# Kernel optimization log

Measured on AMD Instinct MI355X. Metric: run time of the kernel, lower is better.

## Reference

```python
import jax, jax.numpy as jnp
import numpy as np

KS = (3, 3)   # kernel_size
ST = (1, 1)   # stride
PD = (1, 1)   # padding
EPS = 1e-5


def unfold(x):
    """im2col matching torch.nn.Unfold: [B,C,H,W] -> [B, C*kh*kw, L] with (c,kh,kw) channel order, L row-major."""
    kh, kw = KS; sh, sw = ST; ph, pw = PD
    x = jnp.pad(x, ((0, 0), (0, 0), (ph, ph), (pw, pw)))
    B, C, H, W = x.shape
    Ho = (H - kh) // sh + 1
    Wo = (W - kw) // sw + 1
    I = (jnp.arange(Ho) * sh)[:, None, None, None] + jnp.arange(kh)[None, :, None, None]
    J = (jnp.arange(Wo) * sw)[None, None, :, None] + jnp.arange(kw)[None, None, None, :]
    p = x[:, :, I, J]  # [B, C, Ho, kh, Wo, kw]
    return p.transpose(0, 1, 3, 5, 2, 4).reshape(B, C * kh * kw, Ho * Wo)


def fold(cols, x_shape):
    """torch.nn.Fold is exactly the adjoint of Unfold (overlap-add)."""
    _, vjp = jax.vjp(unfold, jnp.zeros(x_shape, cols.dtype))
    return vjp(cols)[0]


def setup_inputs() -> dict:
    key = jax.random.key(0)
    k = jax.random.split(key, 6)
    B, C, H, W = 16, 64, 64, 64
    Cout, K = 64, KS[0] * KS[1]
    return {
        "x_mag": jax.random.uniform(k[0], (B, C, H, W), jnp.float32),
        "x_ang": jax.random.normal(k[1], (B, C, H, W), jnp.float32),
        "w_mag": jax.random.uniform(k[2], (C, K), jnp.float32),
        "w_ang": jax.random.uniform(k[3], (C, K), jnp.float32),
        "w1": jax.random.uniform(k[4], (C, K), jnp.float32),
        "w2": jax.random.uniform(k[5], (Cout, C), jnp.float32),
    }


def reference(x_mag, x_ang, w_mag, w_ang, w1, w2):
    B, C, H, W = x_mag.shape
    K = KS[0] * KS[1]
    Cout = w2.shape[0]
    Ho = (H + 2 * PD[0] - KS[0]) // ST[0] + 1
    Wo = (W + 2 * PD[1] - KS[1]) // ST[1] + 1

    # outer layer: unfold, mix with normalized weights, fold back (overlap-add)
    nws_mag = w_mag ** 2 / jnp.sum(w_mag ** 2)   # _normalize_weights_squared
    nw_ang = w_ang / jnp.sum(w_ang ** 2)         # _normalize_weights
    cm = unfold(x_mag).reshape(B, C, K, -1) + nws_mag[None, :, :, None]
    ca = unfold(x_ang).reshape(B, C, K, -1) * nw_ang[None, :, :, None]
    fm = fold(cm.reshape(B, C * K, -1), (B, C, H, W))
    fa = fold(ca.reshape(B, C * K, -1), (B, C, H, W))

    # helper: second unfold + weighted Frechet-mean reduction
    tbm = unfold(fm).reshape(B, C, K, -1)  # [B,C,K,L]
    tba = unfold(fa).reshape(B, C, K, -1)
    wmm1 = w1 ** 2 / jnp.sum(w1 ** 2, axis=1, keepdims=True)  # row-normalized
    wmm2 = w2 ** 2 / jnp.sum(w2 ** 2, axis=1, keepdims=True)
    wma1 = w1 ** 2 / jnp.sum(w1 ** 2)                          # globally normalized
    wma2 = w2 ** 2 / jnp.sum(w2 ** 2)

    m1 = jnp.einsum('bckl,ck->bcl', jnp.log(tbm + EPS), wmm1)
    out_mag = jnp.exp(jnp.einsum('bcl,oc->bol', m1, wmm2)).reshape(B, Cout, Ho, Wo)
    a1 = jnp.einsum('bckl,ck->bcl', tba, wma1)
    out_ang = jnp.einsum('bcl,oc->bol', a1, wma2).reshape(B, Cout, Ho, Wo)

    # from_polar -> stack (real, imag) on axis 1
    return jnp.stack([out_mag * jnp.cos(out_ang), out_mag * jnp.sin(out_ang)], axis=1)
```

## Files before the change

### kernel.cpp

```cpp
#include <hip/hip_runtime.h>
#include <math.h>

#define NB 16
#define NC 64
#define NL 4096
#define NCOUT 64
#define EPSF 1e-5f
#define LOG_EPSF -11.512925464970229f
#define CC 8
#define NCHUNK 8

#define FMA16(ACC, MV, W) \
  (ACC)[0].x = fmaf((MV).x,(W).x,(ACC)[0].x); (ACC)[0].y = fmaf((MV).y,(W).x,(ACC)[0].y); \
  (ACC)[0].z = fmaf((MV).z,(W).x,(ACC)[0].z); (ACC)[0].w = fmaf((MV).w,(W).x,(ACC)[0].w); \
  (ACC)[1].x = fmaf((MV).x,(W).y,(ACC)[1].x); (ACC)[1].y = fmaf((MV).y,(W).y,(ACC)[1].y); \
  (ACC)[1].z = fmaf((MV).z,(W).y,(ACC)[1].z); (ACC)[1].w = fmaf((MV).w,(W).y,(ACC)[1].w); \
  (ACC)[2].x = fmaf((MV).x,(W).z,(ACC)[2].x); (ACC)[2].y = fmaf((MV).y,(W).z,(ACC)[2].y); \
  (ACC)[2].z = fmaf((MV).z,(W).z,(ACC)[2].z); (ACC)[2].w = fmaf((MV).w,(W).z,(ACC)[2].w); \
  (ACC)[3].x = fmaf((MV).x,(W).w,(ACC)[3].x); (ACC)[3].y = fmaf((MV).y,(W).w,(ACC)[3].y); \
  (ACC)[3].z = fmaf((MV).z,(W).w,(ACC)[3].z); (ACC)[3].w = fmaf((MV).w,(W).w,(ACC)[3].w);

__global__ __launch_bounds__(512, 4) void fused_kernel(
    const float* __restrict__ x_mag, const float* __restrict__ x_ang,
    const float* __restrict__ wm, const float* __restrict__ wa,
    const float* __restrict__ w1, const float* __restrict__ w2,
    float* __restrict__ out)
{
    __shared__ __align__(16) float lfm[CC][4][72];
    __shared__ __align__(16) float fas[CC][4][72];
    __shared__ __align__(16) float m1r[2][CC][2][64];
    __shared__ __align__(16) float a1r[2][CC][2][64];
    __shared__ __align__(16) float w2m[64][68];
    __shared__ float wm1s[64][9], wa1s[64][9];
    __shared__ float smag_s[64][9], tang_s[64][9];
    __shared__ float red[4][8];
    __shared__ __align__(16) float rho[64];

    const int tid  = threadIdx.x;
    const int lane = tid & 63;
    const int wv   = tid >> 6;

    const int bid = (blockIdx.x & 7) * 64 + (blockIdx.x >> 3);
    const int b  = bid >> 5;
    const int i0 = (bid & 31) * 2;

    const int sr = lane >> 4;
    const int j4 = lane & 15;
    const int ir = i0 - 1 + sr;
    const bool ok = ((unsigned)ir < 64u);
    const int irc = ok ? ir : 0;
    const int ci = (ir == 0) ? 0 : ((ir == 63) ? 2 : 1);
    const int kL = ci * 3 + 0, kC = ci * 3 + 1, kR = ci * 3 + 2;
    const float ni = (ci == 1) ? 3.f : 2.f;
    const float nCt = 3.f * ni;
    const float n0 = (j4 == 0)  ? 2.f * ni : nCt;
    const float n3 = (j4 == 15) ? 2.f * ni : nCt;

    const float* spm = x_mag + ((size_t)(b * NC + wv) * NL + irc * 64 + j4 * 4);
    const float* spa = x_ang + ((size_t)(b * NC + wv) * NL + irc * 64 + j4 * 4);

    float4 pfm = *(const float4*)spm;
    float4 pfa = *(const float4*)spa;

    const int mrr = tid >> 8;
    const int o0  = ((tid >> 4) & 15) * 4;
    const int l0  = (tid & 15) * 4;

    float p0 = 0.f, p1 = 0.f, p2 = 0.f;
    {
        float v;
        v = wm[tid]; p0 += v * v;
        v = wa[tid]; p1 += v * v;
        v = w1[tid]; p2 += v * v;
        if (tid < 64) {
            v = wm[tid + 512]; p0 += v * v;
            v = wa[tid + 512]; p1 += v * v;
            v = w1[tid + 512]; p2 += v * v;
        }
    }
    #pragma unroll
    for (int s = 32; s; s >>= 1) {
        p0 += __shfl_down(p0, s); p1 += __shfl_down(p1, s); p2 += __shfl_down(p2, s);
    }
    if (lane == 0) { red[0][wv] = p0; red[1][wv] = p1; red[2][wv] = p2; }

    float sqv[2][4], r2v[2][4];
    float s22p = 0.f;
    #pragma unroll
    for (int k = 0; k < 2; ++k) {
        const int oq = wv + 8 * k;
        #pragma unroll
        for (int n = 0; n < 4; ++n) {
            float v = w2[(oq * 4 + n) * 64 + lane];
            float s = v * v;
            sqv[k][n] = s;
            float rr_ = s;
            rr_ += __shfl_xor(rr_, 1);  rr_ += __shfl_xor(rr_, 2);
            rr_ += __shfl_xor(rr_, 4);  rr_ += __shfl_xor(rr_, 8);
            rr_ += __shfl_xor(rr_, 16); rr_ += __shfl_xor(rr_, 32);
            r2v[k][n] = rr_;
        }
        s22p += r2v[k][0] + r2v[k][1] + r2v[k][2] + r2v[k][3];
    }
    if (lane == 0) red[3][wv] = s22p;
    __syncthreads();
    const float s_wm2 = red[0][0] + red[0][1] + red[0][2] + red[0][3]
                      + red[0][4] + red[0][5] + red[0][6] + red[0][7];
    const float s_wa2 = red[1][0] + red[1][1] + red[1][2] + red[1][3]
                      + red[1][4] + red[1][5] + red[1][6] + red[1][7];
    const float s_w12 = red[2][0] + red[2][1] + red[2][2] + red[2][3]
                      + red[2][4] + red[2][5] + red[2][6] + red[2][7];
    const float inv_s22 = 1.f / (red[3][0] + red[3][1] + red[3][2] + red[3][3]
                               + red[3][4] + red[3][5] + red[3][6] + red[3][7]);

    #pragma unroll
    for (int k = 0; k < 2; ++k) {
        const int oq = wv + 8 * k;
        float4 wmv4;
        wmv4.x = sqv[k][0] / r2v[k][0];
        wmv4.y = sqv[k][1] / r2v[k][1];
        wmv4.z = sqv[k][2] / r2v[k][2];
        wmv4.w = sqv[k][3] / r2v[k][3];
        *(float4*)&w2m[lane][oq * 4] = wmv4;
        if (lane == 0) {
            rho[oq * 4 + 0] = r2v[k][0] * inv_s22;
            rho[oq * 4 + 1] = r2v[k][1] * inv_s22;
            rho[oq * 4 + 2] = r2v[k][2] * inv_s22;
            rho[oq * 4 + 3] = r2v[k][3] * inv_s22;
        }
    }

    if (tid < 64) {
        const int c = tid;
        float q[9]; float r1c = 0.f;
        #pragma unroll
        for (int k = 0; k < 9; ++k) { float v = w1[c * 9 + k]; q[k] = v * v; r1c += q[k]; }
        float inv_r = 1.f / r1c, inv_s = 1.f / s_w12;
        #pragma unroll
        for (int k = 0; k < 9; ++k) { wm1s[c][k] = q[k] * inv_r; wa1s[c][k] = q[k] * inv_s; }
    } else if (tid < 128) {
        const int c = tid - 64;
        float nm[9], na[9];
        const float inv_m = 1.f / s_wm2, inv_a = 1.f / s_wa2;
        #pragma unroll
        for (int k = 0; k < 9; ++k) {
            float v = wm[c * 9 + k];
            nm[k] = v * v * inv_m;
            na[k] = wa[c * 9 + k] * inv_a;
        }
        #pragma unroll
        for (int ci_ = 0; ci_ < 3; ++ci_) {
            #pragma unroll
            for (int cj = 0; cj < 3; ++cj) {
                float sm = 0.f, sa = 0.f;
                #pragma unroll
                for (int ki = 0; ki < 3; ++ki) {
                    bool vi = (ci_ == 0) ? (ki < 2) : ((ci_ == 2) ? (ki > 0) : true);
                    if (!vi) continue;
                    #pragma unroll
                    for (int kj = 0; kj < 3; ++kj) {
                        bool vj = (cj == 0) ? (kj < 2) : ((cj == 2) ? (kj > 0) : true);
                        if (!vj) continue;
                        sm += nm[ki * 3 + kj];
                        sa += na[ki * 3 + kj];
                    }
                }
                smag_s[c][ci_ * 3 + cj] = sm;
                tang_s[c][ci_ * 3 + cj] = sa;
            }
        }
    }
    __syncthreads();

    float4 accm[4], acca[4];
    #pragma unroll
    for (int oi = 0; oi < 4; ++oi) {
        accm[oi].x = accm[oi].y = accm[oi].z = accm[oi].w = 0.f;
        acca[oi].x = acca[oi].y = acca[oi].z = acca[oi].w = 0.f;
    }

    auto do_matmul = [&](int chm, int pp) {
        const int c0 = chm * CC;
        #pragma unroll
        for (int cc = 0; cc < CC; ++cc) {
            float4 mv  = *(const float4*)&m1r[pp][cc][mrr][l0];
            float4 av  = *(const float4*)&a1r[pp][cc][mrr][l0];
            float4 wmv = *(const float4*)&w2m[c0 + cc][o0];
            FMA16(accm, mv, wmv);
            FMA16(acca, av, wmv);
        }
    };

    #pragma unroll 2
    for (int ch = 0; ch < NCHUNK; ++ch) {
        const int p = ch & 1;
        const int cg = ch * CC + wv;

        {
            float4 dm, da;
            if (ok) {
                float sC = smag_s[cg][kC], tC = tang_s[cg][kC];
                float s0 = (j4 == 0)  ? smag_s[cg][kL] : sC;
                float s3 = (j4 == 15) ? smag_s[cg][kR] : sC;
                float t0 = (j4 == 0)  ? tang_s[cg][kL] : tC;
                float t3 = (j4 == 15) ? tang_s[cg][kR] : tC;
                dm.x = __logf(fmaf(n0,  pfm.x, s0) + EPSF);
                dm.y = __logf(fmaf(nCt, pfm.y, sC) + EPSF);
                dm.z = __logf(fmaf(nCt, pfm.z, sC) + EPSF);
                dm.w = __logf(fmaf(n3,  pfm.w, s3) + EPSF);
                da.x = pfa.x * t0; da.y = pfa.y * tC;
                da.z = pfa.z * tC; da.w = pfa.w * t3;
            } else {
                dm.x = dm.y = dm.z = dm.w = LOG_EPSF;
                da.x = da.y = da.z = da.w = 0.f;
            }
            *(float4*)&lfm[wv][sr][4 + j4 * 4] = dm;
            *(float4*)&fas[wv][sr][4 + j4 * 4] = da;
            if (j4 == 0)  { lfm[wv][sr][3]  = LOG_EPSF; fas[wv][sr][3]  = 0.f; }
            if (j4 == 15) { lfm[wv][sr][68] = LOG_EPSF; fas[wv][sr][68] = 0.f; }
        }

        if (ch + 1 < NCHUNK) {
            pfm = *(const float4*)(spm + (size_t)(ch + 1) * CC * NL);
            pfa = *(const float4*)(spa + (size_t)(ch + 1) * CC * NL);
        }

        if (ch > 0) do_matmul(ch - 1, p ^ 1);

        {
            float mres0 = 0.f, mres1 = 0.f, ares0 = 0.f, ares1 = 0.f;
            #pragma unroll
            for (int r_ = 0; r_ < 4; ++r_) {
                float l0v = lfm[wv][r_][lane + 3];
                float l1v = lfm[wv][r_][lane + 4];
                float l2v = lfm[wv][r_][lane + 5];
                float a0v = fas[wv][r_][lane + 3];
                float a1v = fas[wv][r_][lane + 4];
                float a2v = fas[wv][r_][lane + 5];
                if (r_ < 3) {
                    mres0 = fmaf(wm1s[cg][r_ * 3 + 0], l0v, mres0);
                    mres0 = fmaf(wm1s[cg][r_ * 3 + 1], l1v, mres0);
                    mres0 = fmaf(wm1s[cg][r_ * 3 + 2], l2v, mres0);
                    ares0 = fmaf(wa1s[cg][r_ * 3 + 0], a0v, ares0);
                    ares0 = fmaf(wa1s[cg][r_ * 3 + 1], a1v, ares0);
                    ares0 = fmaf(wa1s[cg][r_ * 3 + 2], a2v, ares0);
                }
                if (r_ > 0) {
                    const int ki = r_ - 1;
                    mres1 = fmaf(wm1s[cg][ki * 3 + 0], l0v, mres1);
                    mres1 = fmaf(wm1s[cg][ki * 3 + 1], l1v, mres1);
                    mres1 = fmaf(wm1s[cg][ki * 3 + 2], l2v, mres1);
                    ares1 = fmaf(wa1s[cg][ki * 3 + 0], a0v, ares1);
                    ares1 = fmaf(wa1s[cg][ki * 3 + 1], a1v, ares1);
                    ares1 = fmaf(wa1s[cg][ki * 3 + 2], a2v, ares1);
                }
            }
            m1r[p][wv][0][lane] = mres0;
            m1r[p][wv][1][lane] = mres1;
            a1r[p][wv][0][lane] = ares0;
            a1r[p][wv][1][lane] = ares1;
        }
        __syncthreads();
    }
    do_matmul(NCHUNK - 1, 1);

    const float4 rh4 = *(const float4*)&rho[o0];
    acca[0].x *= rh4.x; acca[0].y *= rh4.x; acca[0].z *= rh4.x; acca[0].w *= rh4.x;
    acca[1].x *= rh4.y; acca[1].y *= rh4.y; acca[1].z *= rh4.y; acca[1].w *= rh4.y;
    acca[2].x *= rh4.z; acca[2].y *= rh4.z; acca[2].z *= rh4.z; acca[2].w *= rh4.z;
    acca[3].x *= rh4.w; acca[3].y *= rh4.w; acca[3].z *= rh4.w; acca[3].w *= rh4.w;

    #pragma unroll
    for (int oi = 0; oi < 4; ++oi) {
        float4 am = accm[oi], aa = acca[oi];
        float4 oc, os;
        float ex;
        ex = __expf(am.x); oc.x = ex * __cosf(aa.x); os.x = ex * __sinf(aa.x);
        ex = __expf(am.y); oc.y = ex * __cosf(aa.y); os.y = ex * __sinf(aa.y);
        ex = __expf(am.z); oc.z = ex * __cosf(aa.z); os.z = ex * __sinf(aa.z);
        ex = __expf(am.w); oc.w = ex * __cosf(aa.w); os.w = ex * __sinf(aa.w);
        size_t gi = ((size_t)(b * 2) * NCOUT + o0 + oi) * NL + (size_t)(i0 + mrr) * 64 + l0;
        *(float4*)&out[gi] = oc;
        *(float4*)&out[gi + (size_t)NCOUT * NL] = os;
    }
}

extern "C" void kernel_launch(void* const* d_in, const int* in_sizes, int n_in,
                              void* d_out, int out_size, void* d_ws, size_t ws_size,
                              hipStream_t stream) {
    const float* x_mag = (const float*)d_in[0];
    const float* x_ang = (const float*)d_in[1];
    const float* w_mag = (const float*)d_in[2];
    const float* w_ang = (const float*)d_in[3];
    const float* w1    = (const float*)d_in[4];
    const float* w2    = (const float*)d_in[5];
    float* out = (float*)d_out;

    fused_kernel<<<NB * 32, 512, 0, stream>>>(x_mag, x_ang, w_mag, w_ang, w1, w2, out);
}
```

Measured before the change: 42.59 us.

## Process one output row per block with 256 threads and raise matmul wave priority

```diff
diff --git a/kernel.cpp b/kernel.cpp
--- a/kernel.cpp
+++ b/kernel.cpp
@@ -7,8 +7,8 @@
 #define NCOUT 64
 #define EPSF 1e-5f
 #define LOG_EPSF -11.512925464970229f
-#define CC 8
-#define NCHUNK 8
+#define CC 4
+#define NCHUNK 16
 
 #define FMA16(ACC, MV, W) \
   (ACC)[0].x = fmaf((MV).x,(W).x,(ACC)[0].x); (ACC)[0].y = fmaf((MV).y,(W).x,(ACC)[0].y); \
@@ -20,34 +20,35 @@
   (ACC)[3].x = fmaf((MV).x,(W).w,(ACC)[3].x); (ACC)[3].y = fmaf((MV).y,(W).w,(ACC)[3].y); \
   (ACC)[3].z = fmaf((MV).z,(W).w,(ACC)[3].z); (ACC)[3].w = fmaf((MV).w,(W).w,(ACC)[3].w);
 
-__global__ __launch_bounds__(512, 4) void fused_kernel(
+__global__ __launch_bounds__(256, 4) void fused_kernel(
     const float* __restrict__ x_mag, const float* __restrict__ x_ang,
     const float* __restrict__ wm, const float* __restrict__ wa,
     const float* __restrict__ w1, const float* __restrict__ w2,
     float* __restrict__ out)
 {
-    __shared__ __align__(16) float lfm[CC][4][72];
-    __shared__ __align__(16) float fas[CC][4][72];
-    __shared__ __align__(16) float m1r[2][CC][2][64];
-    __shared__ __align__(16) float a1r[2][CC][2][64];
+    __shared__ __align__(16) float lfm[CC][3][72];
+    __shared__ __align__(16) float fas[CC][3][72];
+    __shared__ __align__(16) float m1r[2][CC][64];
+    __shared__ __align__(16) float a1r[2][CC][64];
     __shared__ __align__(16) float w2m[64][68];
     __shared__ float wm1s[64][9], wa1s[64][9];
     __shared__ float smag_s[64][9], tang_s[64][9];
-    __shared__ float red[4][8];
+    __shared__ float red[4][4];
     __shared__ __align__(16) float rho[64];
 
     const int tid  = threadIdx.x;
     const int lane = tid & 63;
     const int wv   = tid >> 6;
 
-    const int bid = (blockIdx.x & 7) * 64 + (blockIdx.x >> 3);
-    const int b  = bid >> 5;
-    const int i0 = (bid & 31) * 2;
+    const int bid = (blockIdx.x & 7) * 128 + (blockIdx.x >> 3);
+    const int b  = bid >> 6;
+    const int iy = bid & 63;
 
     const int sr = lane >> 4;
     const int j4 = lane & 15;
-    const int ir = i0 - 1 + sr;
-    const bool ok = ((unsigned)ir < 64u);
+    const bool act = (sr < 3);
+    const int ir = iy - 1 + sr;
+    const bool ok = act && ((unsigned)ir < 64u);
     const int irc = ok ? ir : 0;
     const int ci = (ir == 0) ? 0 : ((ir == 63) ? 2 : 1);
     const int kL = ci * 3 + 0, kC = ci * 3 + 1, kR = ci * 3 + 2;
@@ -59,19 +60,18 @@
     const float* spm = x_mag + ((size_t)(b * NC + wv) * NL + irc * 64 + j4 * 4);
     const float* spa = x_ang + ((size_t)(b * NC + wv) * NL + irc * 64 + j4 * 4);
 
-    float4 pfm = *(const float4*)spm;
-    float4 pfa = *(const float4*)spa;
-
-    const int mrr = tid >> 8;
-    const int o0  = ((tid >> 4) & 15) * 4;
-    const int l0  = (tid & 15) * 4;
+    float4 pfm, pfa;
+    if (act) { pfm = *(const float4*)spm; pfa = *(const float4*)spa; }
+
+    const int o0 = (tid >> 4) * 4;
+    const int l0 = (tid & 15) * 4;
 
     float p0 = 0.f, p1 = 0.f, p2 = 0.f;
     {
         float v;
-        v = wm[tid]; p0 += v * v;
-        v = wa[tid]; p1 += v * v;
-        v = w1[tid]; p2 += v * v;
+        v = wm[tid];       p0 += v * v;  v = wm[tid + 256]; p0 += v * v;
+        v = wa[tid];       p1 += v * v;  v = wa[tid + 256]; p1 += v * v;
+        v = w1[tid];       p2 += v * v;  v = w1[tid + 256]; p2 += v * v;
         if (tid < 64) {
             v = wm[tid + 512]; p0 += v * v;
             v = wa[tid + 512]; p1 += v * v;
@@ -84,11 +84,11 @@
     }
     if (lane == 0) { red[0][wv] = p0; red[1][wv] = p1; red[2][wv] = p2; }
 
-    float sqv[2][4], r2v[2][4];
+    float sqv[4][4], r2v[4][4];
     float s22p = 0.f;
     #pragma unroll
-    for (int k = 0; k < 2; ++k) {
-        const int oq = wv + 8 * k;
+    for (int k = 0; k < 4; ++k) {
+        const int oq = wv + 4 * k;
         #pragma unroll
         for (int n = 0; n < 4; ++n) {
             float v = w2[(oq * 4 + n) * 64 + lane];
@@ -104,18 +104,14 @@
     }
     if (lane == 0) red[3][wv] = s22p;
     __syncthreads();
-    const float s_wm2 = red[0][0] + red[0][1] + red[0][2] + red[0][3]
-                      + red[0][4] + red[0][5] + red[0][6] + red[0][7];
-    const float s_wa2 = red[1][0] + red[1][1] + red[1][2] + red[1][3]
-                      + red[1][4] + red[1][5] + red[1][6] + red[1][7];
-    const float s_w12 = red[2][0] + red[2][1] + red[2][2] + red[2][3]
-                      + red[2][4] + red[2][5] + red[2][6] + red[2][7];
-    const float inv_s22 = 1.f / (red[3][0] + red[3][1] + red[3][2] + red[3][3]
-                               + red[3][4] + red[3][5] + red[3][6] + red[3][7]);
-
-    #pragma unroll
-    for (int k = 0; k < 2; ++k) {
-        const int oq = wv + 8 * k;
+    const float s_wm2 = red[0][0] + red[0][1] + red[0][2] + red[0][3];
+    const float s_wa2 = red[1][0] + red[1][1] + red[1][2] + red[1][3];
+    const float s_w12 = red[2][0] + red[2][1] + red[2][2] + red[2][3];
+    const float inv_s22 = 1.f / (red[3][0] + red[3][1] + red[3][2] + red[3][3]);
+
+    #pragma unroll
+    for (int k = 0; k < 4; ++k) {
+        const int oq = wv + 4 * k;
         float4 wmv4;
         wmv4.x = sqv[k][0] / r2v[k][0];
         wmv4.y = sqv[k][1] / r2v[k][1];
@@ -181,14 +177,16 @@
 
     auto do_matmul = [&](int chm, int pp) {
         const int c0 = chm * CC;
+        __builtin_amdgcn_s_setprio(1);
         #pragma unroll
         for (int cc = 0; cc < CC; ++cc) {
-            float4 mv  = *(const float4*)&m1r[pp][cc][mrr][l0];
-            float4 av  = *(const float4*)&a1r[pp][cc][mrr][l0];
+            float4 mv  = *(const float4*)&m1r[pp][cc][l0];
+            float4 av  = *(const float4*)&a1r[pp][cc][l0];
             float4 wmv = *(const float4*)&w2m[c0 + cc][o0];
             FMA16(accm, mv, wmv);
             FMA16(acca, av, wmv);
         }
+        __builtin_amdgcn_s_setprio(0);
     };
 
     #pragma unroll 2
@@ -196,7 +194,7 @@
         const int p = ch & 1;
         const int cg = ch * CC + wv;
 
-        {
+        if (act) {
             float4 dm, da;
             if (ok) {
                 float sC = smag_s[cg][kC], tC = tang_s[cg][kC];
@@ -220,7 +218,7 @@
             if (j4 == 15) { lfm[wv][sr][68] = LOG_EPSF; fas[wv][sr][68] = 0.f; }
         }
 
-        if (ch + 1 < NCHUNK) {
+        if (act && (ch + 1 < NCHUNK)) {
             pfm = *(const float4*)(spm + (size_t)(ch + 1) * CC * NL);
             pfa = *(const float4*)(spa + (size_t)(ch + 1) * CC * NL);
         }
@@ -228,37 +226,18 @@
         if (ch > 0) do_matmul(ch - 1, p ^ 1);
 
         {
-            float mres0 = 0.f, mres1 = 0.f, ares0 = 0.f, ares1 = 0.f;
+            float mres = 0.f, ares = 0.f;
             #pragma unroll
-            for (int r_ = 0; r_ < 4; ++r_) {
-                float l0v = lfm[wv][r_][lane + 3];
-                float l1v = lfm[wv][r_][lane + 4];
-                float l2v = lfm[wv][r_][lane + 5];
-                float a0v = fas[wv][r_][lane + 3];
-                float a1v = fas[wv][r_][lane + 4];
-                float a2v = fas[wv][r_][lane + 5];
-                if (r_ < 3) {
-                    mres0 = fmaf(wm1s[cg][r_ * 3 + 0], l0v, mres0);
-                    mres0 = fmaf(wm1s[cg][r_ * 3 + 1], l1v, mres0);
-                    mres0 = fmaf(wm1s[cg][r_ * 3 + 2], l2v, mres0);
-                    ares0 = fmaf(wa1s[cg][r_ * 3 + 0], a0v, ares0);
-                    ares0 = fmaf(wa1s[cg][r_ * 3 + 1], a1v, ares0);
-                    ares0 = fmaf(wa1s[cg][r_ * 3 + 2], a2v, ares0);
-                }
-                if (r_ > 0) {
-                    const int ki = r_ - 1;
-                    mres1 = fmaf(wm1s[cg][ki * 3 + 0], l0v, mres1);
-                    mres1 = fmaf(wm1s[cg][ki * 3 + 1], l1v, mres1);
-                    mres1 = fmaf(wm1s[cg][ki * 3 + 2], l2v, mres1);
-                    ares1 = fmaf(wa1s[cg][ki * 3 + 0], a0v, ares1);
-                    ares1 = fmaf(wa1s[cg][ki * 3 + 1], a1v, ares1);
-                    ares1 = fmaf(wa1s[cg][ki * 3 + 2], a2v, ares1);
-                }
+            for (int r_ = 0; r_ < 3; ++r_) {
+                mres = fmaf(wm1s[cg][r_ * 3 + 0], lfm[wv][r_][lane + 3], mres);
+                mres = fmaf(wm1s[cg][r_ * 3 + 1], lfm[wv][r_][lane + 4], mres);
+                mres = fmaf(wm1s[cg][r_ * 3 + 2], lfm[wv][r_][lane + 5], mres);
+                ares = fmaf(wa1s[cg][r_ * 3 + 0], fas[wv][r_][lane + 3], ares);
+                ares = fmaf(wa1s[cg][r_ * 3 + 1], fas[wv][r_][lane + 4], ares);
+                ares = fmaf(wa1s[cg][r_ * 3 + 2], fas[wv][r_][lane + 5], ares);
             }
-            m1r[p][wv][0][lane] = mres0;
-            m1r[p][wv][1][lane] = mres1;
-            a1r[p][wv][0][lane] = ares0;
-            a1r[p][wv][1][lane] = ares1;
+            m1r[p][wv][lane] = mres;
+            a1r[p][wv][lane] = ares;
         }
         __syncthreads();
     }
@@ -279,7 +258,7 @@
         ex = __expf(am.y); oc.y = ex * __cosf(aa.y); os.y = ex * __sinf(aa.y);
         ex = __expf(am.z); oc.z = ex * __cosf(aa.z); os.z = ex * __sinf(aa.z);
         ex = __expf(am.w); oc.w = ex * __cosf(aa.w); os.w = ex * __sinf(aa.w);
-        size_t gi = ((size_t)(b * 2) * NCOUT + o0 + oi) * NL + (size_t)(i0 + mrr) * 64 + l0;
+        size_t gi = ((size_t)(b * 2) * NCOUT + o0 + oi) * NL + (size_t)iy * 64 + l0;
         *(float4*)&out[gi] = oc;
         *(float4*)&out[gi + (size_t)NCOUT * NL] = os;
     }
@@ -296,5 +275,5 @@
     const float* w2    = (const float*)d_in[5];
     float* out = (float*)d_out;
 
-    fused_kernel<<<NB * 32, 512, 0, stream>>>(x_mag, x_ang, w_mag, w_ang, w1, w2, out);
+    fused_kernel<<<NB * 64, 256, 0, stream>>>(x_mag, x_ang, w_mag, w_ang, w1, w2, out);
 }
```

New measurement: 43.87 us. 3.0% more time.

## Halve block to 256 threads, 8x4 output tile per thread, compute w1 weights inline

Applied to the files above, without the earlier changes.

```diff
diff --git a/kernel.cpp b/kernel.cpp
--- a/kernel.cpp
+++ b/kernel.cpp
@@ -7,8 +7,8 @@
 #define NCOUT 64
 #define EPSF 1e-5f
 #define LOG_EPSF -11.512925464970229f
-#define CC 8
-#define NCHUNK 8
+#define CC 4
+#define NCHUNK 16
 
 #define FMA16(ACC, MV, W) \
   (ACC)[0].x = fmaf((MV).x,(W).x,(ACC)[0].x); (ACC)[0].y = fmaf((MV).y,(W).x,(ACC)[0].y); \
@@ -20,7 +20,7 @@
   (ACC)[3].x = fmaf((MV).x,(W).w,(ACC)[3].x); (ACC)[3].y = fmaf((MV).y,(W).w,(ACC)[3].y); \
   (ACC)[3].z = fmaf((MV).z,(W).w,(ACC)[3].z); (ACC)[3].w = fmaf((MV).w,(W).w,(ACC)[3].w);
 
-__global__ __launch_bounds__(512, 4) void fused_kernel(
+__global__ __launch_bounds__(256, 2) void fused_kernel(
     const float* __restrict__ x_mag, const float* __restrict__ x_ang,
     const float* __restrict__ wm, const float* __restrict__ wa,
     const float* __restrict__ w1, const float* __restrict__ w2,
@@ -31,9 +31,8 @@
     __shared__ __align__(16) float m1r[2][CC][2][64];
     __shared__ __align__(16) float a1r[2][CC][2][64];
     __shared__ __align__(16) float w2m[64][68];
-    __shared__ float wm1s[64][9], wa1s[64][9];
     __shared__ float smag_s[64][9], tang_s[64][9];
-    __shared__ float red[4][8];
+    __shared__ float red[4][4];
     __shared__ __align__(16) float rho[64];
 
     const int tid  = threadIdx.x;
@@ -62,16 +61,16 @@
     float4 pfm = *(const float4*)spm;
     float4 pfa = *(const float4*)spa;
 
-    const int mrr = tid >> 8;
-    const int o0  = ((tid >> 4) & 15) * 4;
+    const int mrr = tid >> 7;
+    const int o0  = ((tid >> 4) & 7) * 8;
     const int l0  = (tid & 15) * 4;
 
     float p0 = 0.f, p1 = 0.f, p2 = 0.f;
     {
         float v;
-        v = wm[tid]; p0 += v * v;
-        v = wa[tid]; p1 += v * v;
-        v = w1[tid]; p2 += v * v;
+        v = wm[tid];       p0 += v * v;  v = wm[tid + 256]; p0 += v * v;
+        v = wa[tid];       p1 += v * v;  v = wa[tid + 256]; p1 += v * v;
+        v = w1[tid];       p2 += v * v;  v = w1[tid + 256]; p2 += v * v;
         if (tid < 64) {
             v = wm[tid + 512]; p0 += v * v;
             v = wa[tid + 512]; p1 += v * v;
@@ -84,11 +83,11 @@
     }
     if (lane == 0) { red[0][wv] = p0; red[1][wv] = p1; red[2][wv] = p2; }
 
-    float sqv[2][4], r2v[2][4];
+    float sqv[4][4], r2v[4][4];
     float s22p = 0.f;
     #pragma unroll
-    for (int k = 0; k < 2; ++k) {
-        const int oq = wv + 8 * k;
+    for (int k = 0; k < 4; ++k) {
+        const int oq = wv + 4 * k;
         #pragma unroll
         for (int n = 0; n < 4; ++n) {
             float v = w2[(oq * 4 + n) * 64 + lane];
@@ -104,18 +103,15 @@
     }
     if (lane == 0) red[3][wv] = s22p;
     __syncthreads();
-    const float s_wm2 = red[0][0] + red[0][1] + red[0][2] + red[0][3]
-                      + red[0][4] + red[0][5] + red[0][6] + red[0][7];
-    const float s_wa2 = red[1][0] + red[1][1] + red[1][2] + red[1][3]
-                      + red[1][4] + red[1][5] + red[1][6] + red[1][7];
-    const float s_w12 = red[2][0] + red[2][1] + red[2][2] + red[2][3]
-                      + red[2][4] + red[2][5] + red[2][6] + red[2][7];
-    const float inv_s22 = 1.f / (red[3][0] + red[3][1] + red[3][2] + red[3][3]
-                               + red[3][4] + red[3][5] + red[3][6] + red[3][7]);
-
-    #pragma unroll
-    for (int k = 0; k < 2; ++k) {
-        const int oq = wv + 8 * k;
+    const float s_wm2 = red[0][0] + red[0][1] + red[0][2] + red[0][3];
+    const float s_wa2 = red[1][0] + red[1][1] + red[1][2] + red[1][3];
+    const float s_w12 = red[2][0] + red[2][1] + red[2][2] + red[2][3];
+    const float inv_s22 = 1.f / (red[3][0] + red[3][1] + red[3][2] + red[3][3]);
+    const float inv_s12 = 1.f / s_w12;
+
+    #pragma unroll
+    for (int k = 0; k < 4; ++k) {
+        const int oq = wv + 4 * k;
         float4 wmv4;
         wmv4.x = sqv[k][0] / r2v[k][0];
         wmv4.y = sqv[k][1] / r2v[k][1];
@@ -130,15 +126,7 @@
         }
     }
 
-    if (tid < 64) {
-        const int c = tid;
-        float q[9]; float r1c = 0.f;
-        #pragma unroll
-        for (int k = 0; k < 9; ++k) { float v = w1[c * 9 + k]; q[k] = v * v; r1c += q[k]; }
-        float inv_r = 1.f / r1c, inv_s = 1.f / s_w12;
-        #pragma unroll
-        for (int k = 0; k < 9; ++k) { wm1s[c][k] = q[k] * inv_r; wa1s[c][k] = q[k] * inv_s; }
-    } else if (tid < 128) {
+    if (tid >= 64 && tid < 128) {
         const int c = tid - 64;
         float nm[9], na[9];
         const float inv_m = 1.f / s_wm2, inv_a = 1.f / s_wa2;
@@ -170,11 +158,20 @@
             }
         }
     }
+
+    if (j4 == 0)  { lfm[wv][sr][3]  = LOG_EPSF; fas[wv][sr][3]  = 0.f; }
+    if (j4 == 15) { lfm[wv][sr][68] = LOG_EPSF; fas[wv][sr][68] = 0.f; }
+    if (!ok) {
+        float4 sm4; sm4.x = sm4.y = sm4.z = sm4.w = LOG_EPSF;
+        float4 z4;  z4.x = z4.y = z4.z = z4.w = 0.f;
+        *(float4*)&lfm[wv][sr][4 + j4 * 4] = sm4;
+        *(float4*)&fas[wv][sr][4 + j4 * 4] = z4;
+    }
     __syncthreads();
 
-    float4 accm[4], acca[4];
-    #pragma unroll
-    for (int oi = 0; oi < 4; ++oi) {
+    float4 accm[8], acca[8];
+    #pragma unroll
+    for (int oi = 0; oi < 8; ++oi) {
         accm[oi].x = accm[oi].y = accm[oi].z = accm[oi].w = 0.f;
         acca[oi].x = acca[oi].y = acca[oi].z = acca[oi].w = 0.f;
     }
@@ -185,9 +182,12 @@
         for (int cc = 0; cc < CC; ++cc) {
             float4 mv  = *(const float4*)&m1r[pp][cc][mrr][l0];
             float4 av  = *(const float4*)&a1r[pp][cc][mrr][l0];
-            float4 wmv = *(const float4*)&w2m[c0 + cc][o0];
-            FMA16(accm, mv, wmv);
-            FMA16(acca, av, wmv);
+            float4 w0_ = *(const float4*)&w2m[c0 + cc][o0];
+            float4 w1_ = *(const float4*)&w2m[c0 + cc][o0 + 4];
+            FMA16((&accm[0]), mv, w0_);
+            FMA16((&accm[4]), mv, w1_);
+            FMA16((&acca[0]), av, w0_);
+            FMA16((&acca[4]), av, w1_);
         }
     };
 
@@ -196,28 +196,27 @@
         const int p = ch & 1;
         const int cg = ch * CC + wv;
 
-        {
+        const int cgu = __builtin_amdgcn_readfirstlane(cg);
+        const float* w1row = w1 + cgu * 9;
+        float q[9];
+        #pragma unroll
+        for (int k = 0; k < 9; ++k) q[k] = w1row[k];
+
+        if (ok) {
+            float sC = smag_s[cg][kC], tC = tang_s[cg][kC];
+            float s0 = (j4 == 0)  ? smag_s[cg][kL] : sC;
+            float s3 = (j4 == 15) ? smag_s[cg][kR] : sC;
+            float t0 = (j4 == 0)  ? tang_s[cg][kL] : tC;
+            float t3 = (j4 == 15) ? tang_s[cg][kR] : tC;
             float4 dm, da;
-            if (ok) {
-                float sC = smag_s[cg][kC], tC = tang_s[cg][kC];
-                float s0 = (j4 == 0)  ? smag_s[cg][kL] : sC;
-                float s3 = (j4 == 15) ? smag_s[cg][kR] : sC;
-                float t0 = (j4 == 0)  ? tang_s[cg][kL] : tC;
-                float t3 = (j4 == 15) ? tang_s[cg][kR] : tC;
-                dm.x = __logf(fmaf(n0,  pfm.x, s0) + EPSF);
-                dm.y = __logf(fmaf(nCt, pfm.y, sC) + EPSF);
-                dm.z = __logf(fmaf(nCt, pfm.z, sC) + EPSF);
-                dm.w = __logf(fmaf(n3,  pfm.w, s3) + EPSF);
-                da.x = pfa.x * t0; da.y = pfa.y * tC;
-                da.z = pfa.z * tC; da.w = pfa.w * t3;
-            } else {
-                dm.x = dm.y = dm.z = dm.w = LOG_EPSF;
-                da.x = da.y = da.z = da.w = 0.f;
-            }
+            dm.x = __logf(fmaf(n0,  pfm.x, s0) + EPSF);
+            dm.y = __logf(fmaf(nCt, pfm.y, sC) + EPSF);
+            dm.z = __logf(fmaf(nCt, pfm.z, sC) + EPSF);
+            dm.w = __logf(fmaf(n3,  pfm.w, s3) + EPSF);
+            da.x = pfa.x * t0; da.y = pfa.y * tC;
+            da.z = pfa.z * tC; da.w = pfa.w * t3;
             *(float4*)&lfm[wv][sr][4 + j4 * 4] = dm;
             *(float4*)&fas[wv][sr][4 + j4 * 4] = da;
-            if (j4 == 0)  { lfm[wv][sr][3]  = LOG_EPSF; fas[wv][sr][3]  = 0.f; }
-            if (j4 == 15) { lfm[wv][sr][68] = LOG_EPSF; fas[wv][sr][68] = 0.f; }
         }
 
         if (ch + 1 < NCHUNK) {
@@ -226,6 +225,11 @@
         }
 
         if (ch > 0) do_matmul(ch - 1, p ^ 1);
+
+        #pragma unroll
+        for (int k = 0; k < 9; ++k) q[k] = q[k] * q[k];
+        const float r1c = ((q[0] + q[1]) + (q[2] + q[3])) + ((q[4] + q[5]) + (q[6] + q[7])) + q[8];
+        const float inv_r1 = 1.f / r1c;
 
         {
             float mres0 = 0.f, mres1 = 0.f, ares0 = 0.f, ares1 = 0.f;
@@ -238,40 +242,47 @@
                 float a1v = fas[wv][r_][lane + 4];
                 float a2v = fas[wv][r_][lane + 5];
                 if (r_ < 3) {
-                    mres0 = fmaf(wm1s[cg][r_ * 3 + 0], l0v, mres0);
-                    mres0 = fmaf(wm1s[cg][r_ * 3 + 1], l1v, mres0);
-                    mres0 = fmaf(wm1s[cg][r_ * 3 + 2], l2v, mres0);
-                    ares0 = fmaf(wa1s[cg][r_ * 3 + 0], a0v, ares0);
-                    ares0 = fmaf(wa1s[cg][r_ * 3 + 1], a1v, ares0);
-                    ares0 = fmaf(wa1s[cg][r_ * 3 + 2], a2v, ares0);
+                    mres0 = fmaf(q[r_ * 3 + 0], l0v, mres0);
+                    mres0 = fmaf(q[r_ * 3 + 1], l1v, mres0);
+                    mres0 = fmaf(q[r_ * 3 + 2], l2v, mres0);
+                    ares0 = fmaf(q[r_ * 3 + 0], a0v, ares0);
+                    ares0 = fmaf(q[r_ * 3 + 1], a1v, ares0);
+                    ares0 = fmaf(q[r_ * 3 + 2], a2v, ares0);
                 }
                 if (r_ > 0) {
                     const int ki = r_ - 1;
-                    mres1 = fmaf(wm1s[cg][ki * 3 + 0], l0v, mres1);
-                    mres1 = fmaf(wm1s[cg][ki * 3 + 1], l1v, mres1);
-                    mres1 = fmaf(wm1s[cg][ki * 3 + 2], l2v, mres1);
-                    ares1 = fmaf(wa1s[cg][ki * 3 + 0], a0v, ares1);
-                    ares1 = fmaf(wa1s[cg][ki * 3 + 1], a1v, ares1);
-                    ares1 = fmaf(wa1s[cg][ki * 3 + 2], a2v, ares1);
+                    mres1 = fmaf(q[ki * 3 + 0], l0v, mres1);
+                    mres1 = fmaf(q[ki * 3 + 1], l1v, mres1);
+                    mres1 = fmaf(q[ki * 3 + 2], l2v, mres1);
+                    ares1 = fmaf(q[ki * 3 + 0], a0v, ares1);
+                    ares1 = fmaf(q[ki * 3 + 1], a1v, ares1);
+                    ares1 = fmaf(q[ki * 3 + 2], a2v, ares1);
                 }
             }
-            m1r[p][wv][0][lane] = mres0;
-            m1r[p][wv][1][lane] = mres1;
-            a1r[p][wv][0][lane] = ares0;
-            a1r[p][wv][1][lane] = ares1;
+            m1r[p][wv][0][lane] = mres0 * inv_r1;
+            m1r[p][wv][1][lane] = mres1 * inv_r1;
+            a1r[p][wv][0][lane] = ares0 * inv_s12;
+            a1r[p][wv][1][lane] = ares1 * inv_s12;
         }
         __syncthreads();
     }
     do_matmul(NCHUNK - 1, 1);
 
-    const float4 rh4 = *(const float4*)&rho[o0];
-    acca[0].x *= rh4.x; acca[0].y *= rh4.x; acca[0].z *= rh4.x; acca[0].w *= rh4.x;
-    acca[1].x *= rh4.y; acca[1].y *= rh4.y; acca[1].z *= rh4.y; acca[1].w *= rh4.y;
-    acca[2].x *= rh4.z; acca[2].y *= rh4.z; acca[2].z *= rh4.z; acca[2].w *= rh4.z;
-    acca[3].x *= rh4.w; acca[3].y *= rh4.w; acca[3].z *= rh4.w; acca[3].w *= rh4.w;
-
-    #pragma unroll
-    for (int oi = 0; oi < 4; ++oi) {
+    {
+        const float4 rh0 = *(const float4*)&rho[o0];
+        const float4 rh1 = *(const float4*)&rho[o0 + 4];
+        acca[0].x *= rh0.x; acca[0].y *= rh0.x; acca[0].z *= rh0.x; acca[0].w *= rh0.x;
+        acca[1].x *= rh0.y; acca[1].y *= rh0.y; acca[1].z *= rh0.y; acca[1].w *= rh0.y;
+        acca[2].x *= rh0.z; acca[2].y *= rh0.z; acca[2].z *= rh0.z; acca[2].w *= rh0.z;
+        acca[3].x *= rh0.w; acca[3].y *= rh0.w; acca[3].z *= rh0.w; acca[3].w *= rh0.w;
+        acca[4].x *= rh1.x; acca[4].y *= rh1.x; acca[4].z *= rh1.x; acca[4].w *= rh1.x;
+        acca[5].x *= rh1.y; acca[5].y *= rh1.y; acca[5].z *= rh1.y; acca[5].w *= rh1.y;
+        acca[6].x *= rh1.z; acca[6].y *= rh1.z; acca[6].z *= rh1.z; acca[6].w *= rh1.z;
+        acca[7].x *= rh1.w; acca[7].y *= rh1.w; acca[7].z *= rh1.w; acca[7].w *= rh1.w;
+    }
+
+    #pragma unroll
+    for (int oi = 0; oi < 8; ++oi) {
         float4 am = accm[oi], aa = acca[oi];
         float4 oc, os;
         float ex;
@@ -296,5 +307,5 @@
     const float* w2    = (const float*)d_in[5];
     float* out = (float*)d_out;
 
-    fused_kernel<<<NB * 32, 512, 0, stream>>>(x_mag, x_ang, w_mag, w_ang, w1, w2, out);
+    fused_kernel<<<NB * 32, 256, 0, stream>>>(x_mag, x_ang, w_mag, w_ang, w1, w2, out);
 }
```

Result: faster. 39.97 us (-6.1%).
